# Performance work log

Measured on AMD Instinct MI355X. Metric: run time of the kernel, lower is better.

Reference implementation:

```python
import jax, jax.numpy as jnp
import numpy as np


def setup_inputs() -> dict:
    key = jax.random.key(0)
    ks = jax.random.split(key, 5)
    B, S, D_in, D_out, E, R = 4, 1024, 1024, 1024, 8, 16
    x = jax.random.normal(ks[0], (B, S, D_in), dtype=jnp.float32)
    weight = jax.random.normal(ks[1], (D_out, D_in), dtype=jnp.float32) / np.sqrt(D_in)
    gate_w = jax.random.normal(ks[2], (E, D_in), dtype=jnp.float32) / np.sqrt(D_in)
    lora_U = jax.random.normal(ks[3], (E, R, D_in), dtype=jnp.float32) / np.sqrt(D_in)
    lora_V = jax.random.normal(ks[4], (E, D_out, R), dtype=jnp.float32) / np.sqrt(R)
    return {"x": x, "weight": weight, "gate_w": gate_w, "lora_U": lora_U, "lora_V": lora_V}


def reference(x, weight, gate_w, lora_U, lora_V):
    # MoELoRA forward (global_gating=False), lora_alpha=1.0, rank=16
    scaling = 1.0 / lora_U.shape[1]
    B, S, D_in = x.shape
    xt = x.reshape(-1, D_in)                      # (N, D_in), N = B*S
    # per-token softmax gate over experts
    gate = jax.nn.softmax(xt @ gate_w.T, axis=-1)  # (N, E)
    # base term: sum_e gate[n,e] * (W @ x_n) = W @ x_n since gate sums to 1
    base = xt @ weight.T                           # (N, D_out)
    # low-rank expert contributions without materializing (E, D_out, D_in)
    t = jnp.einsum('nh,erh->ner', xt, lora_U)      # (N, E, R)
    lora = jnp.einsum('ne,eor,ner->no', gate, lora_V, t)  # (N, D_out)
    out = base + scaling * lora
    return out.reshape(B, S, -1)
```

## Files before the change

kernel.cpp:

```cpp
#include <hip/hip_runtime.h>
#include <hip/hip_bf16.h>

typedef __attribute__((ext_vector_type(8))) short short8;
typedef __attribute__((ext_vector_type(4))) float f32x4;

#define NTOK 4096
#define DIN  1024
#define DOUT 1024
#define KTOT 1152
#define XLD  1152
#define TLDS 200

__device__ __forceinline__ unsigned short f2bf(float f) {
    __hip_bfloat16 h = __float2bfloat16(f);
    return __builtin_bit_cast(unsigned short, h);
}

__device__ __forceinline__ void gload16(const void* g, void* l) {
    __builtin_amdgcn_global_load_lds((const __attribute__((address_space(1))) void*)g,
                                     (__attribute__((address_space(3))) void*)l, 16, 0, 0);
}

__device__ __forceinline__ uint4 pack2(float4 v0, float4 v1) {
    union { unsigned short u[8]; uint4 q; } pk;
    pk.u[0] = f2bf(v0.x); pk.u[1] = f2bf(v0.y); pk.u[2] = f2bf(v0.z); pk.u[3] = f2bf(v0.w);
    pk.u[4] = f2bf(v1.x); pk.u[5] = f2bf(v1.y); pk.u[6] = f2bf(v1.z); pk.u[7] = f2bf(v1.w);
    return pk.q;
}

__device__ __forceinline__ uint4 pack8(const float* s) {
    return pack2(*(const float4*)s, *(const float4*)(s + 4));
}

__global__ __launch_bounds__(256) void k_cvtuw(const float* __restrict__ lora_U,
                                               const float* __restrict__ gate_w,
                                               const float* __restrict__ w,
                                               const float* __restrict__ lora_V,
                                               __hip_bfloat16* __restrict__ Ucat,
                                               __hip_bfloat16* __restrict__ Wcat) {
    int b = blockIdx.x;
    if (b < 96) {
        int idx = b * 256 + threadIdx.x;
        int r = idx >> 7, g = idx & 127;
        uint4 q = make_uint4(0u, 0u, 0u, 0u);
        if (r < 128)      q = pack8(lora_U + (size_t)r * DIN + g * 8);
        else if (r < 136) q = pack8(gate_w + (size_t)(r - 128) * DIN + g * 8);
        *(uint4*)(Ucat + (size_t)r * DIN + g * 8) = q;
    } else {
        int idx = (b - 96) * 256 + threadIdx.x;
        int o = idx / 144, g = idx - o * 144;
        const float* s;
        if (g < 128) s = w + (size_t)o * DIN + g * 8;
        else {
            int i0 = (g - 128) * 8;
            int e = i0 >> 4, r = i0 & 15;
            s = lora_V + (size_t)e * (DOUT * 16) + (size_t)o * 16 + r;
        }
        *(uint4*)(Wcat + (size_t)o * KTOT + g * 8) = pack8(s);
    }
}

__global__ __launch_bounds__(256) void k_gemm1f(const float* __restrict__ x,
                                                const __hip_bfloat16* __restrict__ Ucat,
                                                __hip_bfloat16* __restrict__ Xcat) {
    __shared__ char smem[53248];
    float (*Tsm)[TLDS] = (float(*)[TLDS])smem;

    const int t = threadIdx.x, lane = t & 63, wid = t >> 6;
    const int row0 = blockIdx.x * 16;
    const int l7 = lane & 7, l8 = lane >> 3, l15 = lane & 15, l16 = lane >> 4;
    const int scol = ((l7 ^ l8) << 3);

    f32x4 acc[3];
#pragma unroll
    for (int n = 0; n < 3; ++n) acc[n] = (f32x4){0.f, 0.f, 0.f, 0.f};

    const int ar = (t & 127) >> 3;
    const int ac8 = (t & 7) * 8;
    const int abyte = ar * 128 + (((t & 7) ^ (ar & 7)) << 4);

    int boff[3];
#pragma unroll
    for (int n = 0; n < 3; ++n) boff[n] = (wid * 48 + n * 16 + l15) * 128;
    const int aoff = l15 * 128;
    int sw[2];
#pragma unroll
    for (int ks = 0; ks < 2; ++ks) sw[ks] = (((ks * 4 + l16) ^ l7) << 4);

    if (t < 128) {
        uint4 q = pack8(x + (size_t)(row0 + ar) * DIN + 0 + ac8);
        *(uint4*)(smem + 0 * 2048 + abyte) = q;
        *(uint4*)(Xcat + (size_t)(row0 + ar) * XLD + 0 + ac8) = q;
    }
#pragma unroll
    for (int i = 0; i < 6; ++i) {
        int cj = wid * 6 + i;
        gload16(Ucat + (size_t)(cj * 8 + l8) * DIN + 0 + scol,
                smem + 4096 + cj * 1024);
    }
    __syncthreads();

    int cur = 0;
    for (int kt = 0; kt < 16; ++kt) {
        const bool hasNext = kt < 15;
        const int k1 = (kt + 1) << 6;
        float4 f0, f1;
        if (hasNext && t < 128) {
            const float* s = x + (size_t)(row0 + ar) * DIN + k1 + ac8;
            f0 = *(const float4*)s; f1 = *(const float4*)(s + 4);
        }
        if (hasNext) {
#pragma unroll
            for (int i = 0; i < 6; ++i) {
                int cj = wid * 6 + i;
                gload16(Ucat + (size_t)(cj * 8 + l8) * DIN + k1 + scol,
                        smem + 4096 + (cur ^ 1) * 24576 + cj * 1024);
            }
        }
        const char* Ab = smem + cur * 2048;
        const char* Bb = smem + 4096 + cur * 24576;
#pragma unroll
        for (int ks = 0; ks < 2; ++ks) {
            short8 af = *(const short8*)(Ab + aoff + sw[ks]);
#pragma unroll
            for (int n = 0; n < 3; ++n) {
                short8 bf = *(const short8*)(Bb + boff[n] + sw[ks]);
                acc[n] = __builtin_amdgcn_mfma_f32_16x16x32_bf16(af, bf, acc[n], 0, 0, 0);
            }
        }
        if (hasNext && t < 128) {
            uint4 q = pack2(f0, f1);
            *(uint4*)(smem + (cur ^ 1) * 2048 + abyte) = q;
            *(uint4*)(Xcat + (size_t)(row0 + ar) * XLD + k1 + ac8) = q;
        }
        __syncthreads();
        cur ^= 1;
    }

#pragma unroll
    for (int n = 0; n < 3; ++n)
#pragma unroll
        for (int j = 0; j < 4; ++j)
            Tsm[l16 * 4 + j][wid * 48 + n * 16 + l15] = acc[n][j];
    __syncthreads();

    if (t < 128) {
        const int tok = t >> 3, e = t & 7;
        float l[8];
#pragma unroll
        for (int i = 0; i < 8; ++i) l[i] = Tsm[tok][128 + i];
        float m = l[0];
#pragma unroll
        for (int i = 1; i < 8; ++i) m = fmaxf(m, l[i]);
        float s = 0.f;
#pragma unroll
        for (int i = 0; i < 8; ++i) s += __expf(l[i] - m);
        const float g = __expf(l[e] - m) / s * 0.0625f;
        union { unsigned short u[16]; uint4 q[2]; } pk;
#pragma unroll
        for (int jj = 0; jj < 16; ++jj) pk.u[jj] = f2bf(g * Tsm[tok][e * 16 + jj]);
        uint4* dst = (uint4*)(Xcat + (size_t)(row0 + tok) * XLD + 1024 + e * 16);
        dst[0] = pk.q[0]; dst[1] = pk.q[1];
    }
}

__global__ __launch_bounds__(256) void k_gemm2(const __hip_bfloat16* __restrict__ A,
                                               const __hip_bfloat16* __restrict__ B,
                                               float* __restrict__ out) {
    __shared__ char smem[49152];
    const int b = blockIdx.x;
    const int xcd = b & 7, j = b >> 3;
    const int bx = xcd * 4 + (j & 3), by = j >> 2;
    const int row0 = bx * 128, col0 = by * 64;

    const int t = threadIdx.x, lane = t & 63, wid = t >> 6;
    const int wr = wid >> 1, wc = wid & 1;
    const int l7 = lane & 7, l8 = lane >> 3, l15 = lane & 15, l16 = lane >> 4;
    const int scol = ((l7 ^ l8) << 3);

    f32x4 zf = {0.f, 0.f, 0.f, 0.f};
    f32x4 acc[4][2];
#pragma unroll
    for (int m = 0; m < 4; ++m)
#pragma unroll
        for (int n = 0; n < 2; ++n) acc[m][n] = zf;

    int aoff[4], boff[2], sw[2];
#pragma unroll
    for (int m = 0; m < 4; ++m) aoff[m] = (wr * 64 + m * 16 + l15) * 128;
#pragma unroll
    for (int n = 0; n < 2; ++n) boff[n] = (wc * 32 + n * 16 + l15) * 128;
#pragma unroll
    for (int ks = 0; ks < 2; ++ks) sw[ks] = (((ks * 4 + l16) ^ l7) << 4);

#define G2_STAGE(buf, kt)                                                      \
    {                                                                          \
        const int k0_ = (kt) << 6;                                             \
        _Pragma("unroll")                                                      \
        for (int i = 0; i < 4; ++i) {                                          \
            int ci = wid * 4 + i;                                              \
            gload16(A + (size_t)(row0 + ci * 8 + l8) * XLD + k0_ + scol,       \
                    smem + (buf) * 16384 + ci * 1024);                         \
        }                                                                      \
        _Pragma("unroll")                                                      \
        for (int i = 0; i < 2; ++i) {                                          \
            int cj = wid * 2 + i;                                              \
            gload16(B + (size_t)(col0 + cj * 8 + l8) * KTOT + k0_ + scol,      \
                    smem + 32768 + (buf) * 8192 + cj * 1024);                  \
        }                                                                      \
    }

#define G2_COMP(buf)                                                           \
    {                                                                          \
        const char* Ab = smem + (buf) * 16384;                                 \
        const char* Bb = smem + 32768 + (buf) * 8192;                          \
        _Pragma("unroll")                                                      \
        for (int ks = 0; ks < 2; ++ks) {                                       \
            short8 af[4], bf[2];                                               \
            _Pragma("unroll")                                                  \
            for (int m = 0; m < 4; ++m)                                        \
                af[m] = *(const short8*)(Ab + aoff[m] + sw[ks]);               \
            _Pragma("unroll")                                                  \
            for (int n = 0; n < 2; ++n)                                        \
                bf[n] = *(const short8*)(Bb + boff[n] + sw[ks]);               \
            _Pragma("unroll")                                                  \
            for (int m = 0; m < 4; ++m)                                        \
                _Pragma("unroll")                                              \
                for (int n = 0; n < 2; ++n)                                    \
                    acc[m][n] = __builtin_amdgcn_mfma_f32_16x16x32_bf16(       \
                        af[m], bf[n], acc[m][n], 0, 0, 0);                     \
        }                                                                      \
    }

    G2_STAGE(0, 0);
    __syncthreads();
    int cur = 0;
    for (int kt = 0; kt < 17; ++kt) {
        G2_STAGE(cur ^ 1, kt + 1);
        G2_COMP(cur);
        __syncthreads();
        cur ^= 1;
    }
    G2_COMP(cur);

#pragma unroll
    for (int m = 0; m < 4; ++m)
#pragma unroll
        for (int n = 0; n < 2; ++n)
#pragma unroll
            for (int jj = 0; jj < 4; ++jj)
                out[(size_t)(row0 + wr * 64 + m * 16 + l16 * 4 + jj) * DOUT
                    + col0 + wc * 32 + n * 16 + l15] = acc[m][n][jj];
#undef G2_STAGE
#undef G2_COMP
}

extern "C" void kernel_launch(void* const* d_in, const int* in_sizes, int n_in,
                              void* d_out, int out_size, void* d_ws, size_t ws_size,
                              hipStream_t stream) {
    const float* x      = (const float*)d_in[0];
    const float* weight = (const float*)d_in[1];
    const float* gate_w = (const float*)d_in[2];
    const float* lora_U = (const float*)d_in[3];
    const float* lora_V = (const float*)d_in[4];
    float* out = (float*)d_out;

    char* ws = (char*)d_ws;
    __hip_bfloat16* Xcat = (__hip_bfloat16*)ws;
    __hip_bfloat16* Ucat = (__hip_bfloat16*)(ws + 9437184);
    __hip_bfloat16* Wcat = (__hip_bfloat16*)(ws + 9437184 + 393216);

    k_cvtuw<<<672, 256, 0, stream>>>(lora_U, gate_w, weight, lora_V, Ucat, Wcat);
    k_gemm1f<<<256, 256, 0, stream>>>(x, Ucat, Xcat);
    k_gemm2<<<512, 256, 0, stream>>>(Xcat, Wcat, out);
}
```

Measured before the change: 41.13 us.

## Move x bf16 conversion into prep kernel and pipeline GEMMs with explicit vmcnt waits

The fp32-to-bf16 conversion of x moves out of the first GEMM and into the prep conversion kernel, which now writes Xcat directly. The first GEMM then loads its A fragments straight from global bf16 into registers, double-buffered, instead of staging them through LDS. Both GEMMs replace __syncthreads with explicit s_waitcnt vmcnt counts plus raw s_barrier so outstanding async LDS loads can overlap compute. This trades a separate full pass over x (extra launch work and an extra read/write of Xcat) for a lighter GEMM1, and relies on hand-tuned vmcnt values being correct.

```diff
diff --git a/kernel.cpp b/kernel.cpp
--- a/kernel.cpp
+++ b/kernel.cpp
@@ -21,33 +21,36 @@
                                      (__attribute__((address_space(3))) void*)l, 16, 0, 0);
 }
 
-__device__ __forceinline__ uint4 pack2(float4 v0, float4 v1) {
+__device__ __forceinline__ uint4 pack8(const float* s) {
+    float4 v0 = *(const float4*)s, v1 = *(const float4*)(s + 4);
     union { unsigned short u[8]; uint4 q; } pk;
     pk.u[0] = f2bf(v0.x); pk.u[1] = f2bf(v0.y); pk.u[2] = f2bf(v0.z); pk.u[3] = f2bf(v0.w);
     pk.u[4] = f2bf(v1.x); pk.u[5] = f2bf(v1.y); pk.u[6] = f2bf(v1.z); pk.u[7] = f2bf(v1.w);
     return pk.q;
 }
 
-__device__ __forceinline__ uint4 pack8(const float* s) {
-    return pack2(*(const float4*)s, *(const float4*)(s + 4));
-}
-
-__global__ __launch_bounds__(256) void k_cvtuw(const float* __restrict__ lora_U,
+__global__ __launch_bounds__(256) void k_cvtuw(const float* __restrict__ x,
+                                               const float* __restrict__ lora_U,
                                                const float* __restrict__ gate_w,
                                                const float* __restrict__ w,
                                                const float* __restrict__ lora_V,
+                                               __hip_bfloat16* __restrict__ Xcat,
                                                __hip_bfloat16* __restrict__ Ucat,
                                                __hip_bfloat16* __restrict__ Wcat) {
     int b = blockIdx.x;
-    if (b < 96) {
+    if (b < 2048) {
         int idx = b * 256 + threadIdx.x;
+        int n = idx >> 7, g = idx & 127;
+        *(uint4*)(Xcat + (size_t)n * XLD + g * 8) = pack8(x + (size_t)n * DIN + g * 8);
+    } else if (b < 2144) {
+        int idx = (b - 2048) * 256 + threadIdx.x;
         int r = idx >> 7, g = idx & 127;
         uint4 q = make_uint4(0u, 0u, 0u, 0u);
         if (r < 128)      q = pack8(lora_U + (size_t)r * DIN + g * 8);
         else if (r < 136) q = pack8(gate_w + (size_t)(r - 128) * DIN + g * 8);
         *(uint4*)(Ucat + (size_t)r * DIN + g * 8) = q;
     } else {
-        int idx = (b - 96) * 256 + threadIdx.x;
+        int idx = (b - 2144) * 256 + threadIdx.x;
         int o = idx / 144, g = idx - o * 144;
         const float* s;
         if (g < 128) s = w + (size_t)o * DIN + g * 8;
@@ -60,10 +63,10 @@
     }
 }
 
-__global__ __launch_bounds__(256) void k_gemm1f(const float* __restrict__ x,
+__global__ __launch_bounds__(256) void k_gemm1f(const __hip_bfloat16* __restrict__ Xc,
                                                 const __hip_bfloat16* __restrict__ Ucat,
                                                 __hip_bfloat16* __restrict__ Xcat) {
-    __shared__ char smem[53248];
+    __shared__ char smem[49152];
     float (*Tsm)[TLDS] = (float(*)[TLDS])smem;
 
     const int t = threadIdx.x, lane = t & 63, wid = t >> 6;
@@ -75,66 +78,53 @@
 #pragma unroll
     for (int n = 0; n < 3; ++n) acc[n] = (f32x4){0.f, 0.f, 0.f, 0.f};
 
-    const int ar = (t & 127) >> 3;
-    const int ac8 = (t & 7) * 8;
-    const int abyte = ar * 128 + (((t & 7) ^ (ar & 7)) << 4);
-
     int boff[3];
 #pragma unroll
     for (int n = 0; n < 3; ++n) boff[n] = (wid * 48 + n * 16 + l15) * 128;
-    const int aoff = l15 * 128;
     int sw[2];
 #pragma unroll
     for (int ks = 0; ks < 2; ++ks) sw[ks] = (((ks * 4 + l16) ^ l7) << 4);
 
-    if (t < 128) {
-        uint4 q = pack8(x + (size_t)(row0 + ar) * DIN + 0 + ac8);
-        *(uint4*)(smem + 0 * 2048 + abyte) = q;
-        *(uint4*)(Xcat + (size_t)(row0 + ar) * XLD + 0 + ac8) = q;
-    }
+    const __hip_bfloat16* arow = Xc + (size_t)(row0 + l15) * XLD + l16 * 8;
+    short8 areg[2][2];
+
 #pragma unroll
     for (int i = 0; i < 6; ++i) {
         int cj = wid * 6 + i;
-        gload16(Ucat + (size_t)(cj * 8 + l8) * DIN + 0 + scol,
-                smem + 4096 + cj * 1024);
-    }
-    __syncthreads();
-
-    int cur = 0;
+        gload16(Ucat + (size_t)(cj * 8 + l8) * DIN + 0 + scol, smem + cj * 1024);
+    }
+    areg[0][0] = *(const short8*)(arow + 0);
+    areg[0][1] = *(const short8*)(arow + 32);
+
+#pragma unroll
     for (int kt = 0; kt < 16; ++kt) {
-        const bool hasNext = kt < 15;
-        const int k1 = (kt + 1) << 6;
-        float4 f0, f1;
-        if (hasNext && t < 128) {
-            const float* s = x + (size_t)(row0 + ar) * DIN + k1 + ac8;
-            f0 = *(const float4*)s; f1 = *(const float4*)(s + 4);
-        }
-        if (hasNext) {
+        const int cur = kt & 1;
+        if (kt < 15) {
+            const int k1 = (kt + 1) << 6;
 #pragma unroll
             for (int i = 0; i < 6; ++i) {
                 int cj = wid * 6 + i;
                 gload16(Ucat + (size_t)(cj * 8 + l8) * DIN + k1 + scol,
-                        smem + 4096 + (cur ^ 1) * 24576 + cj * 1024);
+                        smem + (cur ^ 1) * 24576 + cj * 1024);
             }
-        }
-        const char* Ab = smem + cur * 2048;
-        const char* Bb = smem + 4096 + cur * 24576;
+            areg[(kt + 1) & 1][0] = *(const short8*)(arow + k1);
+            areg[(kt + 1) & 1][1] = *(const short8*)(arow + k1 + 32);
+            asm volatile("s_waitcnt vmcnt(10)" ::: "memory");
+        } else {
+            asm volatile("s_waitcnt vmcnt(2)" ::: "memory");
+        }
+        __builtin_amdgcn_s_barrier();
+        const char* Bb = smem + cur * 24576;
 #pragma unroll
         for (int ks = 0; ks < 2; ++ks) {
-            short8 af = *(const short8*)(Ab + aoff + sw[ks]);
+            short8 af = areg[cur][ks];
 #pragma unroll
             for (int n = 0; n < 3; ++n) {
                 short8 bf = *(const short8*)(Bb + boff[n] + sw[ks]);
                 acc[n] = __builtin_amdgcn_mfma_f32_16x16x32_bf16(af, bf, acc[n], 0, 0, 0);
             }
         }
-        if (hasNext && t < 128) {
-            uint4 q = pack2(f0, f1);
-            *(uint4*)(smem + (cur ^ 1) * 2048 + abyte) = q;
-            *(uint4*)(Xcat + (size_t)(row0 + ar) * XLD + k1 + ac8) = q;
-        }
-        __syncthreads();
-        cur ^= 1;
+        __builtin_amdgcn_s_barrier();
     }
 
 #pragma unroll
@@ -233,15 +223,19 @@
     }
 
     G2_STAGE(0, 0);
-    __syncthreads();
     int cur = 0;
-    for (int kt = 0; kt < 17; ++kt) {
-        G2_STAGE(cur ^ 1, kt + 1);
+    for (int kt = 0; kt < 18; ++kt) {
+        if (kt < 17) {
+            G2_STAGE(cur ^ 1, kt + 1);
+            asm volatile("s_waitcnt vmcnt(6)" ::: "memory");
+        } else {
+            asm volatile("s_waitcnt vmcnt(0)" ::: "memory");
+        }
+        __builtin_amdgcn_s_barrier();
         G2_COMP(cur);
-        __syncthreads();
+        __builtin_amdgcn_s_barrier();
         cur ^= 1;
     }
-    G2_COMP(cur);
 
 #pragma unroll
     for (int m = 0; m < 4; ++m)
@@ -270,7 +264,7 @@
     __hip_bfloat16* Ucat = (__hip_bfloat16*)(ws + 9437184);
     __hip_bfloat16* Wcat = (__hip_bfloat16*)(ws + 9437184 + 393216);
 
-    k_cvtuw<<<672, 256, 0, stream>>>(lora_U, gate_w, weight, lora_V, Ucat, Wcat);
-    k_gemm1f<<<256, 256, 0, stream>>>(x, Ucat, Xcat);
+    k_cvtuw<<<2720, 256, 0, stream>>>(x, lora_U, gate_w, weight, lora_V, Xcat, Ucat, Wcat);
+    k_gemm1f<<<256, 256, 0, stream>>>(Xcat, Ucat, Xcat);
     k_gemm2<<<512, 256, 0, stream>>>(Xcat, Wcat, out);
 }
```

Result: faster. 38.31 us (median of 2 runs) (-6.9%).
